# Kernel tuning notes

Measured on AMD Instinct MI355X. Metric: run time of the kernel, lower is better.

Reference implementation:

```python
import jax, jax.numpy as jnp
import numpy as np

N_ENT, N_REL, D, H, N_MID = 4096, 200, 128, 4, 9  # 1 input layer + 9 middle layers + 1 out layer
ALPHA = 0.2
NEG = -9e15


def gat_head(x, adj_mask, W, a):
    # x: [N, Fin], W: [Fin, Fout], a: [2*Fout]
    Wh = x @ W                                   # [N, Fout]
    d = Wh.shape[-1]
    f1 = Wh @ a[:d]                              # [N]
    f2 = Wh @ a[d:]                              # [N]
    e = jax.nn.leaky_relu(f1[:, None] + f2[None, :], ALPHA)  # [N, N]
    e = jnp.where(adj_mask, e, NEG)
    attn = jax.nn.softmax(e, axis=-1)
    return attn @ Wh                             # [N, Fout]


def multihead_concat(x, adj_mask, Ws, As):
    # Ws: [H, Fin, Fout], As: [H, 2*Fout] -> elu(concat over heads) [N, H*Fout]
    heads = jax.vmap(lambda W, a: gat_head(x, adj_mask, W, a))(Ws, As)  # [H, N, Fout]
    N = x.shape[0]
    return jax.nn.elu(jnp.transpose(heads, (1, 0, 2)).reshape(N, -1))


def setup_inputs() -> dict:
    key = jax.random.key(0)
    ks = jax.random.split(key, 12)
    s = 0.1
    return {
        "head": jax.random.randint(ks[0], (4096,), 0, N_ENT),
        "relation": jax.random.randint(ks[1], (4096,), 0, N_REL),
        "adj": jax.random.normal(ks[2], (N_ENT, N_ENT), dtype=jnp.float32),
        "entity_emb": jax.random.normal(ks[3], (N_ENT, D), dtype=jnp.float32) * s,
        "relation_emb": jax.random.normal(ks[4], (N_REL, D), dtype=jnp.float32) * s,
        "W0": jax.random.normal(ks[5], (H, D, D), dtype=jnp.float32) * s,
        "a0": jax.random.normal(ks[6], (H, 2 * D), dtype=jnp.float32) * s,
        "Wm": jax.random.normal(ks[7], (N_MID, H, H * D, D), dtype=jnp.float32) * s,
        "am": jax.random.normal(ks[8], (N_MID, H, 2 * D), dtype=jnp.float32) * s,
        "Wo": jax.random.normal(ks[9], (H * D, D), dtype=jnp.float32) * s,
        "ao": jax.random.normal(ks[10], (2 * D,), dtype=jnp.float32) * s,
    }


def reference(head, relation, adj, entity_emb, relation_emb, W0, a0, Wm, am, Wo, ao):
    adj_mask = adj > 0
    # layer 0: D -> H*D
    x = multihead_concat(entity_emb, adj_mask, W0, a0)
    # 9 middle layers: H*D -> H*D (identical shapes -> scan)
    def step(x, params):
        Ws, As = params
        return multihead_concat(x, adj_mask, Ws, As), None
    x, _ = jax.lax.scan(step, x, (Wm, am))
    # output layer: single head H*D -> D, elu applied after
    x = jax.nn.elu(gat_head(x, adj_mask, Wo, ao))
    head_relation_combined = entity_emb[head] + relation_emb[relation]
    return (x, head_relation_combined)
```

## Files before the change

kernel.cpp:

```cpp
#include <hip/hip_runtime.h>

typedef unsigned short u16;
typedef short bf16x8 __attribute__((ext_vector_type(8)));
typedef float f32x4 __attribute__((ext_vector_type(4)));

__device__ __forceinline__ float bf2f(unsigned v) { return __uint_as_float(v << 16); }
__device__ __forceinline__ u16 f2bf(float f) {
    unsigned u = __float_as_uint(f);
    return (u16)((u + 0x7fffu + ((u >> 16) & 1u)) >> 16);
}

__device__ __forceinline__ void gload_lds16(const void* g, void* l) {
    __builtin_amdgcn_global_load_lds(
        (const __attribute__((address_space(1))) unsigned int*)g,
        (__attribute__((address_space(3))) unsigned int*)l, 16, 0, 0);
}


__global__ __launch_bounds__(256) void k_mask(const float* __restrict__ adj,
                                              unsigned* __restrict__ mask) {
    int w = blockIdx.x * 256 + threadIdx.x;
    const float4* q = (const float4*)(adj + (size_t)w * 32);
    unsigned bits = 0u;
#pragma unroll
    for (int i = 0; i < 8; i++) {
        float4 v = q[i];
        if (v.x > 0.f) bits |= (1u << (i * 4 + 0));
        if (v.y > 0.f) bits |= (1u << (i * 4 + 1));
        if (v.z > 0.f) bits |= (1u << (i * 4 + 2));
        if (v.w > 0.f) bits |= (1u << (i * 4 + 3));
    }
    mask[w] = bits;
}

__global__ void k_trans(const float* __restrict__ in, u16* __restrict__ out, int K) {
    __shared__ float t[32][33];
    const float* src = in + (size_t)blockIdx.z * K * 128;
    u16* dst = out + (size_t)blockIdx.z * K * 128;
    int k0 = blockIdx.x * 32, n0 = blockIdx.y * 32;
    int tx = threadIdx.x, ty = threadIdx.y;
#pragma unroll
    for (int i = 0; i < 32; i += 8) t[ty + i][tx] = src[(size_t)(k0 + ty + i) * 128 + n0 + tx];
    __syncthreads();
#pragma unroll
    for (int i = 0; i < 32; i += 8) dst[(size_t)(n0 + ty + i) * K + k0 + tx] = f2bf(t[tx][ty + i]);
}

__global__ __launch_bounds__(256) void k_cvt(const float* __restrict__ in,
                                             u16* __restrict__ out) {
    int t = blockIdx.x * 256 + threadIdx.x;
    float4 v = ((const float4*)in)[t];
    uint2 o;
    o.x = (unsigned)f2bf(v.x) | ((unsigned)f2bf(v.y) << 16);
    o.y = (unsigned)f2bf(v.z) | ((unsigned)f2bf(v.w) << 16);
    ((uint2*)out)[t] = o;
}

__global__ __launch_bounds__(1024, 4) void k_proj(const u16* __restrict__ X,
                                                  const u16* __restrict__ WT,
                                                  const float* __restrict__ avec,
                                                  u16* __restrict__ WhT,
                                                  float* __restrict__ f1,
                                                  float* __restrict__ f2, int Fin) {
    __shared__ u16 As[2][64 * 32];
    __shared__ u16 Bs[2][128 * 32];
    __shared__ float fpart[4][64][2];
    const int tid = threadIdx.x;
    const int wv = tid >> 6, lane = tid & 63;
    const int rg = wv & 3, cg = wv >> 2;
    const int c = lane & 15, quad = lane >> 4;
    const int bofs = (quad ^ ((c >> 1) & 3)) * 8;
    const int h = blockIdx.y;
    const int j0 = blockIdx.x * 64;
    const u16* Wp = WT + (size_t)h * 128 * Fin;
    const int sgr = ((lane & 3) ^ ((lane >> 3) & 3)) * 8;

#define PROJ_STAGE(buf, kb)                                                              \
    do {                                                                                 \
        if (cg == 0)                                                                     \
            gload_lds16(X + (size_t)(j0 + rg * 16 + (lane >> 2)) * Fin + (kb) + sgr,     \
                        (void*)&As[buf][rg * 16 * 32]);                                  \
        else if (cg <= 2)                                                                \
            gload_lds16(Wp + (size_t)((cg - 1) * 64 + rg * 16 + (lane >> 2)) * Fin + (kb) + sgr, \
                        (void*)&Bs[buf][((cg - 1) * 64 + rg * 16) * 32]);                \
    } while (0)

    PROJ_STAGE(0, 0);
    __syncthreads();

    f32x4 acc[2];
    acc[0] = (f32x4){0.f, 0.f, 0.f, 0.f};
    acc[1] = (f32x4){0.f, 0.f, 0.f, 0.f};

    int it = 0;
    for (int kb = 0; kb < Fin; kb += 32, it++) {
        const int cur = it & 1;
        if (kb + 32 < Fin) PROJ_STAGE(cur ^ 1, kb + 32);
        bf16x8 av = *(const bf16x8*)&As[cur][(rg * 16 + c) * 32 + bofs];
#pragma unroll
        for (int e = 0; e < 2; e++) {
            bf16x8 bv = *(const bf16x8*)&Bs[cur][((cg * 2 + e) * 16 + c) * 32 + bofs];
            acc[e] = __builtin_amdgcn_mfma_f32_16x16x32_bf16(av, bv, acc[e], 0, 0, 0);
        }
        __syncthreads();
    }

    u16* Wo = WhT + (size_t)h * 128 * 4096;
    const float* ah = avec + h * 256;
    float p1[4] = {0, 0, 0, 0}, p2[4] = {0, 0, 0, 0};
#pragma unroll
    for (int e = 0; e < 2; e++) {
        const int n = (cg * 2 + e) * 16 + c;
        float a1 = ah[n];
        float a2 = ah[128 + n];
        u16 w4[4];
#pragma unroll
        for (int r = 0; r < 4; r++) {
            float v = acc[e][r];
            w4[r] = f2bf(v);
            p1[r] += v * a1;
            p2[r] += v * a2;
        }
        uint2 pk;
        pk.x = (unsigned)w4[0] | ((unsigned)w4[1] << 16);
        pk.y = (unsigned)w4[2] | ((unsigned)w4[3] << 16);
        *(uint2*)&Wo[(size_t)n * 4096 + j0 + rg * 16 + quad * 4] = pk;
    }
#pragma unroll
    for (int off = 1; off < 16; off <<= 1) {
#pragma unroll
        for (int r = 0; r < 4; r++) {
            p1[r] += __shfl_xor(p1[r], off);
            p2[r] += __shfl_xor(p2[r], off);
        }
    }
    if (c == 0) {
#pragma unroll
        for (int r = 0; r < 4; r++) {
            fpart[cg][rg * 16 + quad * 4 + r][0] = p1[r];
            fpart[cg][rg * 16 + quad * 4 + r][1] = p2[r];
        }
    }
    __syncthreads();
    if (tid < 64) {
        float s1 = fpart[0][tid][0] + fpart[1][tid][0] + fpart[2][tid][0] + fpart[3][tid][0];
        float s2 = fpart[0][tid][1] + fpart[1][tid][1] + fpart[2][tid][1] + fpart[3][tid][1];
        f1[h * 4096 + j0 + tid] = s1;
        f2[h * 4096 + j0 + tid] = s2;
    }
}

template <bool F32OUT>
__global__ __launch_bounds__(1024, 4) void k_attn(const u16* __restrict__ WhT,
                                                  const float* __restrict__ f1g,
                                                  const float* __restrict__ f2g,
                                                  const unsigned char* __restrict__ maskb,
                                                  void* __restrict__ outp, int ostride) {
    __shared__ float f2s[4096];
    __shared__ unsigned char ms[64 * 528];
    __shared__ u16 Bs[2][4][128 * 32];
    __shared__ float f1s[64];
    __shared__ float lpart[4][64];
    __shared__ float redmax[16];
    __shared__ float red[64 * 132];

    const int tid = threadIdx.x;
    const int wv = tid >> 6, lane = tid & 63;
    const int jg = wv >> 2, rg = wv & 3;
    const int c = lane & 15, quad = lane >> 4;
    const int bofs = (quad ^ ((c >> 1) & 3)) * 8;
    const int sgr = ((lane & 3) ^ ((lane >> 3) & 3)) * 8;
    const int h = blockIdx.y;
    const int i0 = blockIdx.x * 64;
    const float LOG2E = 1.4426950408889634f;
    const float* f1h = f1g + h * 4096;
    const float* f2h = f2g + h * 4096;
    const u16* Wp = WhT + (size_t)h * 128 * 4096;

#define ATTN_STAGE(buf, kb)                                                              \
    do {                                                                                 \
        const int jb_ = jg * 1024 + (kb) * 32;                                           \
        _Pragma("unroll")                                                                \
        for (int e = 0; e < 2; e++)                                                      \
            gload_lds16(Wp + (size_t)(rg * 32 + e * 16 + (lane >> 2)) * 4096 + jb_ + sgr, \
                        (void*)&Bs[buf][jg][(rg * 32 + e * 16) * 32]);                   \
    } while (0)

    float mymax = -3.0e38f;
    {
        float4 v = ((const float4*)f2h)[tid];
        v.x *= LOG2E; v.y *= LOG2E; v.z *= LOG2E; v.w *= LOG2E;
        ((float4*)f2s)[tid] = v;
        mymax = fmaxf(fmaxf(v.x, v.y), fmaxf(v.z, v.w));
    }
    if (tid < 64) f1s[tid] = f1h[i0 + tid] * LOG2E;
    {
        const uint4* msrc = (const uint4*)(maskb + (size_t)i0 * 512);
#pragma unroll
        for (int e = 0; e < 2; e++) {
            int o = tid + e * 1024;
            uint4 v = msrc[o];
            int row = o >> 5, col = o & 31;
            *(uint4*)&ms[row * 528 + col * 16] = v;
        }
    }
    ATTN_STAGE(0, 0);
#pragma unroll
    for (int off = 1; off < 64; off <<= 1) mymax = fmaxf(mymax, __shfl_xor(mymax, off));
    if (lane == 0) redmax[wv] = mymax;
    __syncthreads();
    float F2MAX = redmax[0];
#pragma unroll
    for (int i = 1; i < 16; i++) F2MAX = fmaxf(F2MAX, redmax[i]);

    const int iloc = rg * 16 + c;
    const float rf1 = f1s[iloc];
    const float zb = rf1 + F2MAX;
    const float rm = fmaxf(zb, 0.2f * zb);
    const float Ac = rf1 - rm;
    const float Bc = 0.2f * rf1 - rm;

    f32x4 acc[8];
#pragma unroll
    for (int i = 0; i < 8; i++) acc[i] = (f32x4){0.f, 0.f, 0.f, 0.f};
    float lsum = 0.f;

    for (int kb = 0; kb < 32; kb++) {
        const int cur = kb & 1;
        if (kb < 31) ATTN_STAGE(cur ^ 1, kb + 1);
        const int jb = jg * 1024 + kb * 32;
        const unsigned mb = ms[iloc * 528 + jg * 128 + kb * 4 + quad];
        const float4 fa = *(const float4*)&f2s[jb + quad * 8];
        const float4 fb = *(const float4*)&f2s[jb + quad * 8 + 4];
        const float f2v[8] = {fa.x, fa.y, fa.z, fa.w, fb.x, fb.y, fb.z, fb.w};
        union { bf16x8 v; unsigned u[4]; } af;
#pragma unroll
        for (int t = 0; t < 8; t += 2) {
            float s0 = fmaxf(Ac + f2v[t],     __builtin_fmaf(0.2f, f2v[t],     Bc));
            float s1 = fmaxf(Ac + f2v[t + 1], __builtin_fmaf(0.2f, f2v[t + 1], Bc));
            float p0 = __builtin_amdgcn_exp2f(s0);
            float p1 = __builtin_amdgcn_exp2f(s1);
            unsigned u0 = ((mb >> t) & 1u)       ? (__float_as_uint(p0) & 0xffff0000u) : 0u;
            unsigned u1 = ((mb >> (t + 1)) & 1u) ? (__float_as_uint(p1) & 0xffff0000u) : 0u;
            lsum += __uint_as_float(u0) + __uint_as_float(u1);
            af.u[t >> 1] = (u0 >> 16) | u1;
        }
#pragma unroll
        for (int nt = 0; nt < 8; nt++) {
            bf16x8 bv = *(const bf16x8*)&Bs[cur][jg][(nt * 16 + c) * 32 + bofs];
            acc[nt] = __builtin_amdgcn_mfma_f32_16x16x32_bf16(af.v, bv, acc[nt], 0, 0, 0);
        }
        __syncthreads();
    }

    lsum += __shfl_xor(lsum, 16);
    lsum += __shfl_xor(lsum, 32);
    if (quad == 0) lpart[jg][iloc] = lsum;

#pragma unroll
    for (int g = 0; g < 4; g++) {
        __syncthreads();
        if (jg == g) {
#pragma unroll
            for (int nt = 0; nt < 8; nt++) {
#pragma unroll
                for (int r = 0; r < 4; r++) {
                    int idx = (rg * 16 + quad * 4 + r) * 132 + nt * 16 + c;
                    if (g == 0) red[idx] = acc[nt][r];
                    else        red[idx] += acc[nt][r];
                }
            }
        }
    }
    __syncthreads();

    const int row = tid >> 4, cb = tid & 15;
    const float l = lpart[0][row] + lpart[1][row] + lpart[2][row] + lpart[3][row];
    const float linv = 1.0f / l;
    float vv[8];
#pragma unroll
    for (int t = 0; t < 8; t++) {
        float v = red[row * 132 + cb * 8 + t] * linv;
        vv[t] = v > 0.f ? v : __expf(v) - 1.f;
    }
    const size_t obase = (size_t)(i0 + row) * ostride + h * 128 + cb * 8;
    if (F32OUT) {
        float* op = (float*)outp + obase;
        *(float4*)op = *(float4*)&vv[0];
        *(float4*)(op + 4) = *(float4*)&vv[4];
    } else {
        uint4 o;
        o.x = (unsigned)f2bf(vv[0]) | ((unsigned)f2bf(vv[1]) << 16);
        o.y = (unsigned)f2bf(vv[2]) | ((unsigned)f2bf(vv[3]) << 16);
        o.z = (unsigned)f2bf(vv[4]) | ((unsigned)f2bf(vv[5]) << 16);
        o.w = (unsigned)f2bf(vv[6]) | ((unsigned)f2bf(vv[7]) << 16);
        *(uint4*)((u16*)outp + obase) = o;
    }
}

__global__ __launch_bounds__(256) void k_gather(const int* __restrict__ head,
                                                const int* __restrict__ rel,
                                                const float* __restrict__ ent,
                                                const float* __restrict__ rele,
                                                float* __restrict__ out) {
    int t = blockIdx.x * 256 + threadIdx.x;
    int row = t >> 5, sg = t & 31;
    int hh = head[row], rr = rel[row];
    float4 a = ((const float4*)(ent + (size_t)hh * 128))[sg];
    float4 b = ((const float4*)(rele + (size_t)rr * 128))[sg];
    float4 o;
    o.x = a.x + b.x; o.y = a.y + b.y; o.z = a.z + b.z; o.w = a.w + b.w;
    ((float4*)(out + (size_t)row * 128))[sg] = o;
}

extern "C" void kernel_launch(void* const* d_in, const int* in_sizes, int n_in,
                              void* d_out, int out_size, void* d_ws, size_t ws_size,
                              hipStream_t stream) {
    const int*   head = (const int*)d_in[0];
    const int*   rel  = (const int*)d_in[1];
    const float* adj  = (const float*)d_in[2];
    const float* ent  = (const float*)d_in[3];
    const float* rele = (const float*)d_in[4];
    const float* W0   = (const float*)d_in[5];
    const float* a0   = (const float*)d_in[6];
    const float* Wm   = (const float*)d_in[7];
    const float* am   = (const float*)d_in[8];
    const float* Wo   = (const float*)d_in[9];
    const float* ao   = (const float*)d_in[10];

    char* ws = (char*)d_ws;
    unsigned* mask = (unsigned*)(ws + 0);
    u16* WT0 = (u16*)(ws + 2097152);
    u16* WT5 = (u16*)(ws + 2228224);
    u16* WhT = (u16*)(ws + 7077888);
    float* f1 = (float*)(ws + 11272192);
    float* f2 = (float*)(ws + 11337728);
    u16* xA = (u16*)(ws + 11403264);
    u16* xB = (u16*)(ws + 15597568);
    u16* x0 = (u16*)(ws + 19791872);

    float* out_x = (float*)d_out;
    float* out_comb = out_x + (size_t)4096 * 128;

    k_mask<<<2048, 256, 0, stream>>>(adj, mask);
    k_cvt<<<512, 256, 0, stream>>>(ent, x0);
    k_trans<<<dim3(4, 4, 4), dim3(32, 8), 0, stream>>>(W0, WT0, 128);
    k_trans<<<dim3(16, 4, 36), dim3(32, 8), 0, stream>>>(Wm, WT5, 512);
    k_trans<<<dim3(16, 4, 1), dim3(32, 8), 0, stream>>>(Wo, WT5 + (size_t)36 * 512 * 128, 512);
    k_gather<<<512, 256, 0, stream>>>(head, rel, ent, rele, out_comb);

    k_proj<<<dim3(64, 4), 1024, 0, stream>>>(x0, WT0, a0, WhT, f1, f2, 128);
    k_attn<false><<<dim3(64, 4), 1024, 0, stream>>>(WhT, f1, f2, (const unsigned char*)mask, xA, 512);
    u16 *xc = xA, *xn = xB;
    for (int l = 0; l < 9; l++) {
        k_proj<<<dim3(64, 4), 1024, 0, stream>>>(xc, WT5 + (size_t)l * 4 * 512 * 128,
                                                 am + (size_t)l * 4 * 256, WhT, f1, f2, 512);
        k_attn<false><<<dim3(64, 4), 1024, 0, stream>>>(WhT, f1, f2, (const unsigned char*)mask, xn, 512);
        u16* t = xc; xc = xn; xn = t;
    }
    k_proj<<<dim3(64, 1), 1024, 0, stream>>>(xc, WT5 + (size_t)36 * 512 * 128, ao, WhT, f1, f2, 512);
    k_attn<true><<<dim3(64, 1), 1024, 0, stream>>>(WhT, f1, f2, (const unsigned char*)mask, out_x, 128);
}
```

Before: 653.0 us.

## Factor attention exponentials into per-column and per-row terms to drop inner-loop exp

The exponent of the leaky-ReLU score is split into a per-column factor (exp2 of f2 minus its max, computed for both the positive and the 0.2 slope) and per-row constants. The hot loop then replaces two exp2 calls per pair with a compare, select and multiply against the tabulated values. The 16KB f2 shared array is removed and the table is stored in the existing reduction buffer, which frees shared memory. The trade is an extra 8-byte table read per element and slightly different rounding or underflow behaviour for very negative scores.

```diff
diff --git a/kernel.cpp b/kernel.cpp
--- a/kernel.cpp
+++ b/kernel.cpp
@@ -156,7 +156,6 @@
                                                   const float* __restrict__ f2g,
                                                   const unsigned char* __restrict__ maskb,
                                                   void* __restrict__ outp, int ostride) {
-    __shared__ float f2s[4096];
     __shared__ unsigned char ms[64 * 528];
     __shared__ u16 Bs[2][4][128 * 32];
     __shared__ float f1s[64];
@@ -176,6 +175,7 @@
     const float* f1h = f1g + h * 4096;
     const float* f2h = f2g + h * 4096;
     const u16* Wp = WhT + (size_t)h * 128 * 4096;
+    float* E12 = red;
 
 #define ATTN_STAGE(buf, kb)                                                              \
     do {                                                                                 \
@@ -186,12 +186,17 @@
                         (void*)&Bs[buf][jg][(rg * 32 + e * 16) * 32]);                   \
     } while (0)
 
+    float f2p[8];
     float mymax = -3.0e38f;
     {
-        float4 v = ((const float4*)f2h)[tid];
-        v.x *= LOG2E; v.y *= LOG2E; v.z *= LOG2E; v.w *= LOG2E;
-        ((float4*)f2s)[tid] = v;
-        mymax = fmaxf(fmaxf(v.x, v.y), fmaxf(v.z, v.w));
+        float4 v0 = ((const float4*)f2h)[tid * 2];
+        float4 v1 = ((const float4*)f2h)[tid * 2 + 1];
+        f2p[0] = v0.x * LOG2E; f2p[1] = v0.y * LOG2E;
+        f2p[2] = v0.z * LOG2E; f2p[3] = v0.w * LOG2E;
+        f2p[4] = v1.x * LOG2E; f2p[5] = v1.y * LOG2E;
+        f2p[6] = v1.z * LOG2E; f2p[7] = v1.w * LOG2E;
+#pragma unroll
+        for (int k = 0; k < 8; k++) mymax = fmaxf(mymax, f2p[k]);
     }
     if (tid < 64) f1s[tid] = f1h[i0 + tid] * LOG2E;
     {
@@ -213,33 +218,46 @@
 #pragma unroll
     for (int i = 1; i < 16; i++) F2MAX = fmaxf(F2MAX, redmax[i]);
 
+    {
+        const int j0w = tid * 8;
+#pragma unroll
+        for (int k = 0; k < 8; k += 2) {
+            float d0 = f2p[k] - F2MAX, d1 = f2p[k + 1] - F2MAX;
+            float4 w;
+            w.x = __builtin_amdgcn_exp2f(d0);
+            w.y = __builtin_amdgcn_exp2f(0.2f * d0);
+            w.z = __builtin_amdgcn_exp2f(d1);
+            w.w = __builtin_amdgcn_exp2f(0.2f * d1);
+            *(float4*)&E12[2 * (j0w + k)] = w;
+        }
+    }
+
     const int iloc = rg * 16 + c;
     const float rf1 = f1s[iloc];
     const float zb = rf1 + F2MAX;
     const float rm = fmaxf(zb, 0.2f * zb);
-    const float Ac = rf1 - rm;
-    const float Bc = 0.2f * rf1 - rm;
+    const float C1 = __builtin_amdgcn_exp2f(zb - rm);
+    const float C2 = __builtin_amdgcn_exp2f(0.2f * zb - rm);
+    const float T  = __builtin_amdgcn_exp2f(-zb);
 
     f32x4 acc[8];
 #pragma unroll
     for (int i = 0; i < 8; i++) acc[i] = (f32x4){0.f, 0.f, 0.f, 0.f};
     float lsum = 0.f;
+
+    __syncthreads();
 
     for (int kb = 0; kb < 32; kb++) {
         const int cur = kb & 1;
         if (kb < 31) ATTN_STAGE(cur ^ 1, kb + 1);
-        const int jb = jg * 1024 + kb * 32;
         const unsigned mb = ms[iloc * 528 + jg * 128 + kb * 4 + quad];
-        const float4 fa = *(const float4*)&f2s[jb + quad * 8];
-        const float4 fb = *(const float4*)&f2s[jb + quad * 8 + 4];
-        const float f2v[8] = {fa.x, fa.y, fa.z, fa.w, fb.x, fb.y, fb.z, fb.w};
+        const float* ep = &E12[2 * (jg * 1024 + kb * 32 + quad * 8)];
         union { bf16x8 v; unsigned u[4]; } af;
 #pragma unroll
         for (int t = 0; t < 8; t += 2) {
-            float s0 = fmaxf(Ac + f2v[t],     __builtin_fmaf(0.2f, f2v[t],     Bc));
-            float s1 = fmaxf(Ac + f2v[t + 1], __builtin_fmaf(0.2f, f2v[t + 1], Bc));
-            float p0 = __builtin_amdgcn_exp2f(s0);
-            float p1 = __builtin_amdgcn_exp2f(s1);
+            float4 e = *(const float4*)(ep + 2 * t);
+            float p0 = ((e.x > T) ? C1 : C2) * ((e.x > T) ? e.x : e.y);
+            float p1 = ((e.z > T) ? C1 : C2) * ((e.z > T) ? e.z : e.w);
             unsigned u0 = ((mb >> t) & 1u)       ? (__float_as_uint(p0) & 0xffff0000u) : 0u;
             unsigned u1 = ((mb >> (t + 1)) & 1u) ? (__float_as_uint(p1) & 0xffff0000u) : 0u;
             lsum += __uint_as_float(u0) + __uint_as_float(u1);
```

New measurement: 675.1 us. 3.4% more time.
